# Optimization experiments

Hardware: AMD Instinct MI355X
Metric: run time of the kernel (lower is better)

Reference implementation:

```python
import jax, jax.numpy as jnp
import numpy as np

S = 3072        # total packed tokens
E = 1280        # d_model
H = 20          # encoder_attention_heads
D = E // H      # head_dim = 64
NSEG = 16       # number of packed audio chunks


def setup_inputs() -> dict:
    key = jax.random.key(0)
    ks = jax.random.split(key, 9)
    w = lambda k, shape: (jax.random.normal(k, shape, jnp.float32) * 0.02)
    hidden_states = jax.random.normal(ks[0], (S, E), jnp.float32)
    cu_seqlens = (jnp.arange(NSEG + 1, dtype=jnp.int32) * (S // NSEG))
    return {
        "hidden_states": hidden_states,
        "Wq": w(ks[1], (E, E)), "bq": w(ks[2], (E,)),
        "Wk": w(ks[3], (E, E)),                      # k_proj has no bias
        "Wv": w(ks[4], (E, E)), "bv": w(ks[5], (E,)),
        "Wo": w(ks[6], (E, E)), "bo": w(ks[7], (E,)),
        "cu_seqlens": cu_seqlens,
    }


def reference(hidden_states, Wq, bq, Wk, Wv, bv, Wo, bo, cu_seqlens):
    Sq, Em = hidden_states.shape
    Dh = Em // H
    # projections (torch Linear: x @ W.T + b)
    q = (hidden_states @ Wq.T + bq).reshape(Sq, H, Dh).transpose(1, 0, 2)  # [H,S,D]
    k = (hidden_states @ Wk.T).reshape(Sq, H, Dh).transpose(1, 0, 2)       # [H,S,D]
    v = (hidden_states @ Wv.T + bv).reshape(Sq, H, Dh).transpose(1, 0, 2)  # [H,S,D]
    # block-diagonal additive mask from cu_seqlens (vectorized equivalent of
    # the original Python loop): tokens attend only within their own segment.
    pos = jnp.arange(Sq)
    seg = jnp.searchsorted(cu_seqlens[1:], pos, side="right")              # segment id per token
    same = seg[:, None] == seg[None, :]                                    # [S,S]
    bias = jnp.where(same, 0.0, jnp.finfo(q.dtype).min)
    attn = jnp.einsum("hqd,hkd->hqk", q, k) / np.sqrt(Dh).astype(q.dtype)  # [H,S,S]
    attn = jax.nn.softmax(attn + bias, axis=-1)
    out = jnp.einsum("hqk,hkd->hqd", attn, v)                              # [H,S,D]
    out = out.transpose(1, 0, 2).reshape(Sq, Em)
    return out @ Wo.T + bo
```

## Files before the change

### kernel.cpp

```cpp
#include <hip/hip_runtime.h>
#include <hip/hip_bf16.h>
#include <stdint.h>

#define S_TOK 3072
#define E_DIM 1280
#define H_NUM 20
#define D_HEAD 64
#define NSEG 16

typedef __attribute__((ext_vector_type(8))) short short8;
typedef __attribute__((ext_vector_type(4))) float f32x4;

__device__ __forceinline__ unsigned short f2bf(float f){
  union { float f; unsigned int i; } u; u.f = f;
  unsigned int r = u.i + 0x7FFFu + ((u.i >> 16) & 1u);
  return (unsigned short)(r >> 16);
}

__device__ __forceinline__ void gload_lds16(const void* g, void* l){
  __builtin_amdgcn_global_load_lds((__attribute__((address_space(1))) void*)(g),
                                   (__attribute__((address_space(3))) void*)(l), 16, 0, 0);
}

__global__ void cvt_all(const float* __restrict__ hs,
                        const float* __restrict__ w0, const float* __restrict__ w1,
                        const float* __restrict__ w2,
                        unsigned short* __restrict__ hsb,
                        unsigned short* __restrict__ dqkv,
                        int nHS4, int nW4){
  int i = blockIdx.x * blockDim.x + threadIdx.x;
  const float* src;
  unsigned short* dst;
  size_t sj, dj;
  if (i < nHS4){
    src = hs; dst = hsb; sj = i; dj = i;
  } else {
    int t = i - nHS4;
    int w = t / nW4;
    if (w >= 3) return;
    int j = t - w * nW4;
    src = (w == 0) ? w0 : (w == 1) ? w1 : w2;
    sj = j;
    dst = dqkv; dj = (size_t)w * nW4 + j;
  }
  float4 v = reinterpret_cast<const float4*>(src)[sj];
  ushort4 o;
  o.x = f2bf(v.x); o.y = f2bf(v.y); o.z = f2bf(v.z); o.w = f2bf(v.w);
  reinterpret_cast<ushort4*>(dst)[dj] = o;
}

#define LGKM0 do { asm volatile("s_waitcnt lgkmcnt(0)" ::: "memory");         \
                   __builtin_amdgcn_sched_barrier(0); } while (0)
#define BAR   __builtin_amdgcn_s_barrier()

__global__ __launch_bounds__(512, 2) void gemm_qkv(
    const unsigned short* __restrict__ A,
    const unsigned short* __restrict__ Bp,
    const float* __restrict__ bias0,
    const float* __restrict__ bias1,
    unsigned short* __restrict__ Oq,
    unsigned short* __restrict__ Ok,
    unsigned short* __restrict__ Ov,
    int K)
{
  constexpr int SLOT = (192 + 256) * 64;
  __shared__ __align__(16) unsigned short SH[2 * SLOT];

  const int nwg = gridDim.x;
  const int xcd = blockIdx.x & 7, ix = blockIdx.x >> 3;
  const int wg = xcd * (nwg >> 3) + ix;
  const int st = wg / 20, ii = wg % 20;
  const int bm = (st / 3) * 4 + ii / 5;
  const int bn = (st % 3) * 5 + ii % 5;
  const int row0 = bm * 192, col0 = bn * 256;

  const int tid  = threadIdx.x;
  const int lane = tid & 63;
  const int w    = tid >> 6;
  const int wm   = w >> 2;
  const int wn   = w & 3;

  const f32x4 fz = {0.f, 0.f, 0.f, 0.f};
  f32x4 acc[4][3][2];
#pragma unroll
  for (int qd = 0; qd < 4; ++qd)
#pragma unroll
    for (int m = 0; m < 3; ++m)
#pragma unroll
      for (int n = 0; n < 2; ++n) acc[qd][m][n] = fz;

  auto stA = [&](int t){
    unsigned short* d = SH + (t & 1) * SLOT;
    const unsigned short* g = A + (size_t)row0 * K + (t << 6);
#pragma unroll
    for (int i = 0; i < 3; ++i){
      int s = i * 512 + tid;
      int r = s >> 3, ks = (s & 7) ^ (r & 7);
      gload_lds16(g + (size_t)r * K + ks * 8, d + s * 8);
    }
  };
  auto stB = [&](int h, int t){
    unsigned short* d = SH + (t & 1) * SLOT + 12288 + h * 8192;
    const unsigned short* g = Bp + (size_t)(col0 + h * 128) * K + (t << 6);
#pragma unroll
    for (int i = 0; i < 2; ++i){
      int s = i * 512 + tid;
      int r = s >> 3, ks = (s & 7) ^ (r & 7);
      gload_lds16(g + (size_t)r * K + ks * 8, d + s * 8);
    }
  };

  short8 af[3][2], bf0[2][2], bf1[2][2];
  auto RA = [&](int mh, int db){
    const unsigned short* Ah = SH + db * SLOT;
#pragma unroll
    for (int m = 0; m < 3; ++m){
      int ra = mh * 96 + wm * 48 + m * 16 + (lane & 15);
#pragma unroll
      for (int kk = 0; kk < 2; ++kk){
        int sl = kk * 4 + (lane >> 4);
        af[m][kk] = *reinterpret_cast<const short8*>(&Ah[ra * 64 + ((sl ^ (ra & 7))) * 8]);
      }
    }
  };
  auto RB = [&](int nh, int db, short8 (*bf)[2]){
    const unsigned short* Bb = SH + db * SLOT + 12288;
#pragma unroll
    for (int n = 0; n < 2; ++n){
      int rb = nh * 128 + wn * 32 + n * 16 + (lane & 15);
#pragma unroll
      for (int kk = 0; kk < 2; ++kk){
        int sl = kk * 4 + (lane >> 4);
        bf[n][kk] = *reinterpret_cast<const short8*>(&Bb[rb * 64 + ((sl ^ (rb & 7))) * 8]);
      }
    }
  };

#define MF_Q(QD, BF)                                                          \
  do {                                                                        \
    __builtin_amdgcn_s_setprio(1);                                            \
    _Pragma("unroll")                                                         \
    for (int kk = 0; kk < 2; ++kk)                                            \
      _Pragma("unroll")                                                       \
      for (int m = 0; m < 3; ++m)                                             \
        _Pragma("unroll")                                                     \
        for (int n = 0; n < 2; ++n)                                           \
          acc[QD][m][n] = __builtin_amdgcn_mfma_f32_16x16x32_bf16(            \
              af[m][kk], BF[n][kk], acc[QD][m][n], 0, 0, 0);                  \
    __builtin_amdgcn_s_setprio(0);                                            \
  } while (0)

  const int nk = K >> 6;
  stA(0); stB(0, 0); stB(1, 0);
  for (int t = 0; t < nk; ++t){
    const int db = t & 1;
    const bool nx = (t + 1 < nk);
    asm volatile("s_waitcnt vmcnt(2)" ::: "memory");
    BAR;
    RA(0, db); RB(0, db, bf0);
    if (nx) stA(t + 1);
    LGKM0; MF_Q(0, bf0);
    if (nx) asm volatile("s_waitcnt vmcnt(3)" ::: "memory");
    else    asm volatile("s_waitcnt vmcnt(0)" ::: "memory");
    BAR;
    RB(1, db, bf1);
    if (nx) stB(0, t + 1);
    LGKM0; MF_Q(1, bf1);
    BAR;
    RA(1, db);
    if (nx) stB(1, t + 1);
    LGKM0; MF_Q(2, bf1);
    BAR;
    MF_Q(3, bf0);
  }
  __syncthreads();

  {
    unsigned short* Cs = SH;
    const int CSTR = 264;
    const int mat = col0 / E_DIM;
    const int cc0 = col0 - mat * E_DIM;
    unsigned short* dst = (mat == 0) ? Oq : ((mat == 1) ? Ok : Ov);
    float bb[2][2];
#pragma unroll
    for (int nh = 0; nh < 2; ++nh)
#pragma unroll
      for (int n = 0; n < 2; ++n){
        int cc = cc0 + nh * 128 + wn * 32 + n * 16 + (lane & 15);
        bb[nh][n] = (mat == 0) ? bias0[cc] : (mat == 2 ? bias1[cc] : 0.0f);
      }
#pragma unroll
    for (int ph = 0; ph < 2; ++ph){
#pragma unroll
      for (int q2i = 0; q2i < 2; ++q2i){
        const int qd = ph * 2 + q2i;
        const int nh = (qd >> 1) ^ (qd & 1);
#pragma unroll
        for (int m = 0; m < 3; ++m)
#pragma unroll
          for (int n = 0; n < 2; ++n)
#pragma unroll
            for (int j = 0; j < 4; ++j){
              int rr = wm * 48 + m * 16 + (lane >> 4) * 4 + j;
              int c  = nh * 128 + wn * 32 + n * 16 + (lane & 15);
              Cs[rr * CSTR + c] = f2bf(acc[qd][m][n][j] + bb[nh][n]);
            }
      }
      __syncthreads();
#pragma unroll
      for (int i = 0; i < 6; ++i){
        int tk  = i * 512 + tid;
        int p   = tk / 768;
        int idx = tk - p * 768;
        int rr  = idx >> 3, sq = idx & 7;
        short8 vv = *reinterpret_cast<const short8*>(&Cs[rr * CSTR + p * 64 + sq * 8]);
        int gr = row0 + ph * 96 + rr;
        int hh = (cc0 >> 6) + p;
        *reinterpret_cast<short8*>(&dst[((size_t)hh * S_TOK + gr) * D_HEAD + sq * 8]) = vv;
      }
      __syncthreads();
    }
  }
#undef MF_Q
}

__global__ __launch_bounds__(256, 2) void gemm_out(
    const unsigned short* __restrict__ A,
    const unsigned short* __restrict__ Bp,
    const float* __restrict__ bias0,
    float* __restrict__ Of,
    int K)
{
  constexpr int HS = 64 * 64;
  __shared__ __align__(16) unsigned short SH[8 * HS];

  const int nwg = gridDim.x;
  const int xcd = blockIdx.x & 7, ix = blockIdx.x >> 3;
  const int wg = xcd * (nwg >> 3) + ix;
  const int st = wg / 20, ii = wg % 20;
  const int bm = (st / 2) * 4 + ii / 5;
  const int bn = (st % 2) * 5 + ii % 5;
  const int row0 = bm * 128, col0 = bn * 128;

  const int tid  = threadIdx.x;
  const int lane = tid & 63;
  const int w    = tid >> 6;
  const int wm   = w >> 1;
  const int wn   = w & 1;

  const f32x4 fz = {0.f, 0.f, 0.f, 0.f};
  f32x4 acc[4][2][2];
#pragma unroll
  for (int qd = 0; qd < 4; ++qd)
#pragma unroll
    for (int m = 0; m < 2; ++m)
#pragma unroll
      for (int n = 0; n < 2; ++n) acc[qd][m][n] = fz;

  const int s1 = tid, s2 = 256 + tid;
  const int r1 = s1 >> 3, ks1 = (s1 & 7) ^ (r1 & 7);
  const int r2 = s2 >> 3, ks2 = (s2 & 7) ^ (r2 & 7);

  auto stA = [&](int h, int t){
    unsigned short* d = SH + ((t & 1) * 4 + h) * HS;
    const unsigned short* g = A + (size_t)(row0 + h * 64) * K + (t << 6);
    gload_lds16(g + (size_t)r1 * K + ks1 * 8, d + s1 * 8);
    gload_lds16(g + (size_t)r2 * K + ks2 * 8, d + s2 * 8);
  };
  auto stB = [&](int h, int t){
    unsigned short* d = SH + ((t & 1) * 4 + 2 + h) * HS;
    const unsigned short* g = Bp + (size_t)(col0 + h * 64) * K + (t << 6);
    gload_lds16(g + (size_t)r1 * K + ks1 * 8, d + s1 * 8);
    gload_lds16(g + (size_t)r2 * K + ks2 * 8, d + s2 * 8);
  };

  short8 af[2][2], bf0[2][2], bf1[2][2];
  auto RA = [&](int mh, int db){
    const unsigned short* Ah = SH + (db * 4 + mh) * HS;
#pragma unroll
    for (int m = 0; m < 2; ++m){
      int ra = wm * 32 + m * 16 + (lane & 15);
#pragma unroll
      for (int kk = 0; kk < 2; ++kk){
        int sl = kk * 4 + (lane >> 4);
        af[m][kk] = *reinterpret_cast<const short8*>(&Ah[ra * 64 + ((sl ^ (ra & 7))) * 8]);
      }
    }
  };
  auto RB = [&](int nh, int db, short8 (*bf)[2]){
    const unsigned short* Bh = SH + (db * 4 + 2 + nh) * HS;
#pragma unroll
    for (int n = 0; n < 2; ++n){
      int rb = wn * 32 + n * 16 + (lane & 15);
#pragma unroll
      for (int kk = 0; kk < 2; ++kk){
        int sl = kk * 4 + (lane >> 4);
        bf[n][kk] = *reinterpret_cast<const short8*>(&Bh[rb * 64 + ((sl ^ (rb & 7))) * 8]);
      }
    }
  };

#define MF_Q(QD, BF)                                                          \
  do {                                                                        \
    __builtin_amdgcn_s_setprio(1);                                            \
    _Pragma("unroll")                                                         \
    for (int kk = 0; kk < 2; ++kk)                                            \
      _Pragma("unroll")                                                       \
      for (int m = 0; m < 2; ++m)                                             \
        _Pragma("unroll")                                                     \
        for (int n = 0; n < 2; ++n)                                           \
          acc[QD][m][n] = __builtin_amdgcn_mfma_f32_16x16x32_bf16(            \
              af[m][kk], BF[n][kk], acc[QD][m][n], 0, 0, 0);                  \
    __builtin_amdgcn_s_setprio(0);                                            \
  } while (0)

  const int nk = K >> 6;
  stA(0, 0); stB(0, 0); stB(1, 0); stA(1, 0);
  for (int t = 0; t < nk; ++t){
    const int db = t & 1;
    const bool nx = (t + 1 < nk);
    asm volatile("s_waitcnt vmcnt(4)" ::: "memory");
    BAR;
    RA(0, db); RB(0, db, bf0);
    if (nx) stA(0, t + 1);
    LGKM0; MF_Q(0, bf0);
    if (nx) asm volatile("s_waitcnt vmcnt(4)" ::: "memory");
    else    asm volatile("s_waitcnt vmcnt(2)" ::: "memory");
    BAR;
    RB(1, db, bf1);
    if (nx) stB(0, t + 1);
    LGKM0; MF_Q(1, bf1);
    if (nx) asm volatile("s_waitcnt vmcnt(4)" ::: "memory");
    else    asm volatile("s_waitcnt vmcnt(0)" ::: "memory");
    BAR;
    RA(1, db);
    if (nx) stB(1, t + 1);
    LGKM0; MF_Q(2, bf1);
    BAR;
    if (nx) stA(1, t + 1);
    MF_Q(3, bf0);
  }
  __syncthreads();

  float bc[2][2];
#pragma unroll
  for (int nh = 0; nh < 2; ++nh)
#pragma unroll
    for (int n = 0; n < 2; ++n)
      bc[nh][n] = bias0[col0 + nh * 64 + wn * 32 + n * 16 + (lane & 15)];
#pragma unroll
  for (int qd = 0; qd < 4; ++qd){
    const int mh = qd >> 1;
    const int nh = (qd >> 1) ^ (qd & 1);
#pragma unroll
    for (int m = 0; m < 2; ++m)
#pragma unroll
      for (int n = 0; n < 2; ++n){
        int c = col0 + nh * 64 + wn * 32 + n * 16 + (lane & 15);
#pragma unroll
        for (int j = 0; j < 4; ++j){
          int r = row0 + mh * 64 + wm * 32 + m * 16 + (lane >> 4) * 4 + j;
          Of[(size_t)r * E_DIM + c] = acc[qd][m][n][j] + bc[nh][n];
        }
      }
  }
#undef MF_Q
}

#define VSTR 200
#define PSTR 72
#define ATTN_BLKS (H_NUM * NSEG * 3)
__global__ __launch_bounds__(256, 3) void attn_kernel(
    const unsigned short* __restrict__ Q,
    const unsigned short* __restrict__ Kb,
    const unsigned short* __restrict__ V,
    const int* __restrict__ cu,
    unsigned short* __restrict__ O,
    const float* __restrict__ Wo,
    unsigned short* __restrict__ wob,
    int nW4)
{
  __shared__ __align__(16) unsigned short Vt[64*VSTR];
  __shared__ __align__(16) unsigned short Pw[4][16][PSTR];

  const int bid  = blockIdx.x;
  if (bid >= ATTN_BLKS){
    int i = (bid - ATTN_BLKS) * 256 + threadIdx.x;
    if (i < nW4){
      float4 v = reinterpret_cast<const float4*>(Wo)[i];
      ushort4 o;
      o.x = f2bf(v.x); o.y = f2bf(v.y); o.z = f2bf(v.z); o.w = f2bf(v.w);
      reinterpret_cast<ushort4*>(wob)[i] = o;
    }
    return;
  }
  const int unit = bid / 3;
  const int third= bid - unit*3;
  const int h    = unit >> 4;
  const int seg  = unit & 15;
  const int s0   = cu[seg];
  const int L    = cu[seg + 1] - s0;
  if (L <= 0) return;

  const int tid  = threadIdx.x;
  const int lane = tid & 63;
  const int w    = tid >> 6;
  const int row0g = third*64 + w*16;

  const unsigned short* qh = Q  + (size_t)h * S_TOK * D_HEAD;
  const unsigned short* kh = Kb + (size_t)h * S_TOK * D_HEAD;
  const unsigned short* vh = V  + (size_t)h * S_TOK * D_HEAD;

#pragma unroll
  for (int i = 0; i < 6; ++i){
    int task = i*256 + tid;
    int sr   = task % 192;
    int grp  = task / 192;
    int svr  = s0 + (sr < L ? sr : L - 1);
    short8 vv = *reinterpret_cast<const short8*>(vh + (size_t)svr*64 + grp*8);
#pragma unroll
    for (int j = 0; j < 8; ++j) Vt[(grp*8 + j)*VSTR + sr] = (unsigned short)vv[j];
  }

  short8 qf[2];
#pragma unroll
  for (int kk = 0; kk < 2; ++kk){
    int r  = row0g + (lane & 15);
    int sr = s0 + (r < L ? r : L - 1);
    qf[kk] = *reinterpret_cast<const short8*>(qh + (size_t)sr*64 + kk*32 + (lane >> 4)*8);
  }

  __syncthreads();

  const f32x4 fz = {0.f, 0.f, 0.f, 0.f};
  const float SCL = 0.125f * 1.44269504088896f;

  f32x4 sacc[12];
#pragma unroll
  for (int nt = 0; nt < 12; ++nt) sacc[nt] = fz;

#pragma unroll
  for (int nt = 0; nt < 12; ++nt){
    int rb = nt*16 + (lane & 15);
    int sr = s0 + (rb < L ? rb : L - 1);
    const unsigned short* kr = kh + (size_t)sr*64 + (lane >> 4)*8;
    short8 kf0 = *reinterpret_cast<const short8*>(kr);
    short8 kf1 = *reinterpret_cast<const short8*>(kr + 32);
    sacc[nt] = __builtin_amdgcn_mfma_f32_16x16x32_bf16(qf[0], kf0, sacc[nt], 0, 0, 0);
    sacc[nt] = __builtin_amdgcn_mfma_f32_16x16x32_bf16(qf[1], kf1, sacc[nt], 0, 0, 0);
  }

  float rinv[4];
#pragma unroll
  for (int j = 0; j < 4; ++j){
    float mx = -1e30f;
#pragma unroll
    for (int nt = 0; nt < 12; ++nt){
      int c = nt*16 + (lane & 15);
      float vv = (c < L) ? sacc[nt][j] : -1e30f;
      sacc[nt][j] = vv;
      mx = fmaxf(mx, vv);
    }
    mx = fmaxf(mx, __shfl_xor(mx, 1, 64));
    mx = fmaxf(mx, __shfl_xor(mx, 2, 64));
    mx = fmaxf(mx, __shfl_xor(mx, 4, 64));
    mx = fmaxf(mx, __shfl_xor(mx, 8, 64));
    float sum = 0.f;
#pragma unroll
    for (int nt = 0; nt < 12; ++nt){
      float pp = exp2f((sacc[nt][j] - mx) * SCL);
      sacc[nt][j] = pp;
      sum += pp;
    }
    sum += __shfl_xor(sum, 1, 64);
    sum += __shfl_xor(sum, 2, 64);
    sum += __shfl_xor(sum, 4, 64);
    sum += __shfl_xor(sum, 8, 64);
    rinv[j] = 1.0f / sum;
  }

  f32x4 oacc[4];
#pragma unroll
  for (int nt = 0; nt < 4; ++nt) oacc[nt] = fz;

#pragma unroll
  for (int kk = 0; kk < 6; ++kk){
#pragma unroll
    for (int ntl = 0; ntl < 2; ++ntl){
      int nt = kk*2 + ntl;
#pragma unroll
      for (int j = 0; j < 4; ++j)
        Pw[w][(lane >> 4)*4 + j][ntl*16 + (lane & 15)] = f2bf(sacc[nt][j]);
    }
    short8 pf = *reinterpret_cast<const short8*>(&Pw[w][lane & 15][(lane >> 4)*8]);
#pragma unroll
    for (int nt4 = 0; nt4 < 4; ++nt4){
      int dcol = nt4*16 + (lane & 15);
      short8 vf = *reinterpret_cast<const short8*>(&Vt[dcol*VSTR + kk*32 + (lane >> 4)*8]);
      oacc[nt4] = __builtin_amdgcn_mfma_f32_16x16x32_bf16(pf, vf, oacc[nt4], 0, 0, 0);
    }
  }

#pragma unroll
  for (int nt4 = 0; nt4 < 4; ++nt4)
#pragma unroll
    for (int j = 0; j < 4; ++j)
      Pw[w][(lane >> 4)*4 + j][nt4*16 + (lane & 15)] = f2bf(oacc[nt4][j] * rinv[j]);

  {
    int r = lane >> 2;
    int gr = row0g + r;
    if (gr < L){
#pragma unroll
      for (int part = 0; part < 2; ++part){
        int c0 = (lane & 3)*16 + part*8;
        short8 vv = *reinterpret_cast<const short8*>(&Pw[w][r][c0]);
        *reinterpret_cast<short8*>(&O[(size_t)(s0 + gr) * E_DIM + h*64 + c0]) = vv;
      }
    }
  }
}

extern "C" void kernel_launch(void* const* d_in, const int* in_sizes, int n_in,
                              void* d_out, int out_size, void* d_ws, size_t ws_size,
                              hipStream_t stream)
{
  const float* hs = (const float*)d_in[0];
  const float* Wq = (const float*)d_in[1];
  const float* bq = (const float*)d_in[2];
  const float* Wk = (const float*)d_in[3];
  const float* Wv = (const float*)d_in[4];
  const float* bv = (const float*)d_in[5];
  const float* Wo = (const float*)d_in[6];
  const float* bo = (const float*)d_in[7];
  const int*   cu = (const int*)d_in[8];
  float* out = (float*)d_out;

  unsigned short* p = (unsigned short*)d_ws;
  unsigned short* hsb  = p; p += (size_t)S_TOK * E_DIM;
  unsigned short* wqkv = p; p += (size_t)3 * E_DIM * E_DIM;
  unsigned short* wob  = p; p += (size_t)E_DIM * E_DIM;
  unsigned short* qb   = p; p += (size_t)S_TOK * E_DIM;
  unsigned short* kb   = p; p += (size_t)S_TOK * E_DIM;
  unsigned short* vb   = p; p += (size_t)S_TOK * E_DIM;
  unsigned short* aob  = p; p += (size_t)S_TOK * E_DIM;

  const int nHS4 = S_TOK * E_DIM / 4;
  const int nW4  = E_DIM * E_DIM / 4;
  const int nCvt = nHS4 + 3 * nW4;
  cvt_all<<<(nCvt + 255) / 256, 256, 0, stream>>>(hs, Wq, Wk, Wv, hsb, wqkv, nHS4, nW4);

  gemm_qkv<<<(S_TOK/192) * (3*E_DIM/256), 512, 0, stream>>>(
      hsb, wqkv, bq, bv, qb, kb, vb, E_DIM);

  const int cvtWoBlks = (nW4 + 255) / 256;
  attn_kernel<<<ATTN_BLKS + cvtWoBlks, 256, 0, stream>>>(
      qb, kb, vb, cu, aob, Wo, wob, nW4);

  gemm_out<<<(S_TOK/128) * (E_DIM/128), 256, 0, stream>>>(
      aob, wob, bo, out, E_DIM);
}
```

Measured before the change: 87.19 us.

## Retile output projection GEMM to 64x128 tiles with K=32 double buffering

Replaces the 128x128-tile output GEMM, which had a four-quadrant software pipeline over K=64 steps, with a simpler 64x128 tile using K=32 double-buffered LDS stages and one barrier per step. The grid doubles to 480 workgroups and launch bounds allow four per CU, giving more parallelism and occupancy on a small GEMM. In exchange there is less data reuse per tile, more K iterations with a full vmcnt(0) wait each step, and the finer-grained latency hiding of the old pipeline is gone.

```diff
diff --git a/kernel.cpp b/kernel.cpp
--- a/kernel.cpp
+++ b/kernel.cpp
@@ -224,23 +224,22 @@
 #undef MF_Q
 }
 
-__global__ __launch_bounds__(256, 2) void gemm_out(
+__global__ __launch_bounds__(256, 4) void gemm_out(
     const unsigned short* __restrict__ A,
     const unsigned short* __restrict__ Bp,
     const float* __restrict__ bias0,
     float* __restrict__ Of,
     int K)
 {
-  constexpr int HS = 64 * 64;
-  __shared__ __align__(16) unsigned short SH[8 * HS];
+  constexpr int SLOT = (64 + 128) * 32;
+  __shared__ __align__(16) unsigned short SH[2 * SLOT];
 
   const int nwg = gridDim.x;
   const int xcd = blockIdx.x & 7, ix = blockIdx.x >> 3;
   const int wg = xcd * (nwg >> 3) + ix;
-  const int st = wg / 20, ii = wg % 20;
-  const int bm = (st / 2) * 4 + ii / 5;
-  const int bn = (st % 2) * 5 + ii % 5;
-  const int row0 = bm * 128, col0 = bn * 128;
+  const int bm = wg % 48;
+  const int bn = wg / 48;
+  const int row0 = bm * 64, col0 = bn * 128;
 
   const int tid  = threadIdx.x;
   const int lane = tid & 63;
@@ -249,122 +248,74 @@
   const int wn   = w & 1;
 
   const f32x4 fz = {0.f, 0.f, 0.f, 0.f};
-  f32x4 acc[4][2][2];
-#pragma unroll
-  for (int qd = 0; qd < 4; ++qd)
-#pragma unroll
-    for (int m = 0; m < 2; ++m)
-#pragma unroll
-      for (int n = 0; n < 2; ++n) acc[qd][m][n] = fz;
-
-  const int s1 = tid, s2 = 256 + tid;
-  const int r1 = s1 >> 3, ks1 = (s1 & 7) ^ (r1 & 7);
-  const int r2 = s2 >> 3, ks2 = (s2 & 7) ^ (r2 & 7);
-
-  auto stA = [&](int h, int t){
-    unsigned short* d = SH + ((t & 1) * 4 + h) * HS;
-    const unsigned short* g = A + (size_t)(row0 + h * 64) * K + (t << 6);
-    gload_lds16(g + (size_t)r1 * K + ks1 * 8, d + s1 * 8);
-    gload_lds16(g + (size_t)r2 * K + ks2 * 8, d + s2 * 8);
+  f32x4 acc[2][4];
+#pragma unroll
+  for (int m = 0; m < 2; ++m)
+#pragma unroll
+    for (int n = 0; n < 4; ++n) acc[m][n] = fz;
+
+  auto stage = [&](int buf, int t){
+    unsigned short* base = SH + buf * SLOT;
+    const int k0 = t << 5;
+#pragma unroll
+    for (int i = 0; i < 3; ++i){
+      int s = i * 256 + tid;
+      int r = s >> 2, p = s & 3;
+      int ks = p ^ ((r >> 1) & 3);
+      const unsigned short* g = (r < 64)
+          ? A  + (size_t)(row0 + r) * K + k0 + ks * 8
+          : Bp + (size_t)(col0 + (r - 64)) * K + k0 + ks * 8;
+      gload_lds16(g, base + s * 8);
+    }
   };
-  auto stB = [&](int h, int t){
-    unsigned short* d = SH + ((t & 1) * 4 + 2 + h) * HS;
-    const unsigned short* g = Bp + (size_t)(col0 + h * 64) * K + (t << 6);
-    gload_lds16(g + (size_t)r1 * K + ks1 * 8, d + s1 * 8);
-    gload_lds16(g + (size_t)r2 * K + ks2 * 8, d + s2 * 8);
-  };
-
-  short8 af[2][2], bf0[2][2], bf1[2][2];
-  auto RA = [&](int mh, int db){
-    const unsigned short* Ah = SH + (db * 4 + mh) * HS;
+
+  const int nk = K >> 5;
+  stage(0, 0);
+  int buf = 0;
+  for (int t = 0; t < nk; ++t){
+    asm volatile("s_waitcnt vmcnt(0)" ::: "memory");
+    BAR;
+    if (t + 1 < nk) stage(buf ^ 1, t + 1);
+    const unsigned short* As = SH + buf * SLOT;
+    const unsigned short* Bs = As + 64 * 32;
+    short8 af[2], bf[4];
 #pragma unroll
     for (int m = 0; m < 2; ++m){
       int ra = wm * 32 + m * 16 + (lane & 15);
-#pragma unroll
-      for (int kk = 0; kk < 2; ++kk){
-        int sl = kk * 4 + (lane >> 4);
-        af[m][kk] = *reinterpret_cast<const short8*>(&Ah[ra * 64 + ((sl ^ (ra & 7))) * 8]);
-      }
-    }
-  };
-  auto RB = [&](int nh, int db, short8 (*bf)[2]){
-    const unsigned short* Bh = SH + (db * 4 + 2 + nh) * HS;
-#pragma unroll
-    for (int n = 0; n < 2; ++n){
-      int rb = wn * 32 + n * 16 + (lane & 15);
-#pragma unroll
-      for (int kk = 0; kk < 2; ++kk){
-        int sl = kk * 4 + (lane >> 4);
-        bf[n][kk] = *reinterpret_cast<const short8*>(&Bh[rb * 64 + ((sl ^ (rb & 7))) * 8]);
-      }
-    }
-  };
-
-#define MF_Q(QD, BF)                                                          \
-  do {                                                                        \
-    __builtin_amdgcn_s_setprio(1);                                            \
-    _Pragma("unroll")                                                         \
-    for (int kk = 0; kk < 2; ++kk)                                            \
-      _Pragma("unroll")                                                       \
-      for (int m = 0; m < 2; ++m)                                             \
-        _Pragma("unroll")                                                     \
-        for (int n = 0; n < 2; ++n)                                           \
-          acc[QD][m][n] = __builtin_amdgcn_mfma_f32_16x16x32_bf16(            \
-              af[m][kk], BF[n][kk], acc[QD][m][n], 0, 0, 0);                  \
-    __builtin_amdgcn_s_setprio(0);                                            \
-  } while (0)
-
-  const int nk = K >> 6;
-  stA(0, 0); stB(0, 0); stB(1, 0); stA(1, 0);
-  for (int t = 0; t < nk; ++t){
-    const int db = t & 1;
-    const bool nx = (t + 1 < nk);
-    asm volatile("s_waitcnt vmcnt(4)" ::: "memory");
-    BAR;
-    RA(0, db); RB(0, db, bf0);
-    if (nx) stA(0, t + 1);
-    LGKM0; MF_Q(0, bf0);
-    if (nx) asm volatile("s_waitcnt vmcnt(4)" ::: "memory");
-    else    asm volatile("s_waitcnt vmcnt(2)" ::: "memory");
-    BAR;
-    RB(1, db, bf1);
-    if (nx) stB(0, t + 1);
-    LGKM0; MF_Q(1, bf1);
-    if (nx) asm volatile("s_waitcnt vmcnt(4)" ::: "memory");
-    else    asm volatile("s_waitcnt vmcnt(0)" ::: "memory");
-    BAR;
-    RA(1, db);
-    if (nx) stB(1, t + 1);
-    LGKM0; MF_Q(2, bf1);
-    BAR;
-    if (nx) stA(1, t + 1);
-    MF_Q(3, bf0);
-  }
-  __syncthreads();
-
-  float bc[2][2];
-#pragma unroll
-  for (int nh = 0; nh < 2; ++nh)
-#pragma unroll
-    for (int n = 0; n < 2; ++n)
-      bc[nh][n] = bias0[col0 + nh * 64 + wn * 32 + n * 16 + (lane & 15)];
-#pragma unroll
-  for (int qd = 0; qd < 4; ++qd){
-    const int mh = qd >> 1;
-    const int nh = (qd >> 1) ^ (qd & 1);
+      int sl = lane >> 4;
+      af[m] = *reinterpret_cast<const short8*>(&As[ra * 32 + ((sl ^ ((ra >> 1) & 3))) * 8]);
+    }
+#pragma unroll
+    for (int n = 0; n < 4; ++n){
+      int rb = wn * 64 + n * 16 + (lane & 15);
+      int sl = lane >> 4;
+      bf[n] = *reinterpret_cast<const short8*>(&Bs[rb * 32 + ((sl ^ ((rb >> 1) & 3))) * 8]);
+    }
+    __builtin_amdgcn_s_setprio(1);
 #pragma unroll
     for (int m = 0; m < 2; ++m)
 #pragma unroll
-      for (int n = 0; n < 2; ++n){
-        int c = col0 + nh * 64 + wn * 32 + n * 16 + (lane & 15);
-#pragma unroll
-        for (int j = 0; j < 4; ++j){
-          int r = row0 + mh * 64 + wm * 32 + m * 16 + (lane >> 4) * 4 + j;
-          Of[(size_t)r * E_DIM + c] = acc[qd][m][n][j] + bc[nh][n];
-        }
-      }
-  }
-#undef MF_Q
+      for (int n = 0; n < 4; ++n)
+        acc[m][n] = __builtin_amdgcn_mfma_f32_16x16x32_bf16(af[m], bf[n], acc[m][n], 0, 0, 0);
+    __builtin_amdgcn_s_setprio(0);
+    buf ^= 1;
+  }
+
+  float bc[4];
+#pragma unroll
+  for (int n = 0; n < 4; ++n)
+    bc[n] = bias0[col0 + wn * 64 + n * 16 + (lane & 15)];
+#pragma unroll
+  for (int m = 0; m < 2; ++m)
+#pragma unroll
+    for (int n = 0; n < 4; ++n){
+      int c = col0 + wn * 64 + n * 16 + (lane & 15);
+#pragma unroll
+      for (int j = 0; j < 4; ++j){
+        int r = row0 + wm * 32 + m * 16 + (lane >> 4) * 4 + j;
+        Of[(size_t)r * E_DIM + c] = acc[m][n][j] + bc[n];
+      }
+    }
 }
 
 #define VSTR 200
@@ -557,6 +508,6 @@
   attn_kernel<<<ATTN_BLKS + cvtWoBlks, 256, 0, stream>>>(
       qb, kb, vb, cu, aob, Wo, wob, nW4);
 
-  gemm_out<<<(S_TOK/128) * (E_DIM/128), 256, 0, stream>>>(
+  gemm_out<<<(S_TOK/64) * (E_DIM/128), 256, 0, stream>>>(
       aob, wob, bo, out, E_DIM);
 }
```

New measurement: 90.83 us. 1.04x slower.
